# Kernel tuning notes

Measured on AMD Instinct MI355X. Metric: run time of the kernel, lower is better.

Reference implementation:

```python
import jax, jax.numpy as jnp
import numpy as np

MAXDISP = 320
NEG_SLOPE = 0.2


def _lrelu(x):
    return jnp.where(x >= 0, x, NEG_SLOPE * x)


def _conv(x, w, b, stride):
    # NCHW conv, VALID padding (torch Conv2d with padding=0)
    y = jax.lax.conv_general_dilated(x, w, window_strides=stride, padding='VALID',
                                     dimension_numbers=('NCHW', 'OIHW', 'NCHW'))
    return y + b[None, :, None, None]


def _tile_pair(fl, fr, wa, ba, wb, bb):
    # left: 4x4 conv stride (4,4); right: ZeroPad2d((0,3,0,0)) then stride (4,1)
    tl = _lrelu(_conv(_lrelu(_conv(fl, wa, ba, (4, 4))), wb, bb, (1, 1)))
    frp = jnp.pad(fr, ((0, 0), (0, 0), (0, 0), (0, 3)))
    tr = _lrelu(_conv(_lrelu(_conv(frp, wa, ba, (4, 1))), wb, bb, (1, 1)))
    return tl, tr


def _calc_init_disp(fl, fr, D):
    # fl: [B,C,h,w4], fr: [B,C,h,w] with w = 4*w4.
    # grid_sample(nearest, align_corners=True) with integer coords reduces to
    # exact gather at right column index 4*j - d, zero outside (padding_mode=zeros).
    B, C, h, w4 = fl.shape
    w = fr.shape[3]
    j = jnp.arange(w4)
    d = jnp.arange(D)
    idx = 4 * j[None, :] - d[:, None]              # [D, w4]
    valid = idx >= 0                               # only left edge can go OOB
    idxc = jnp.clip(idx, 0, w - 1)
    fr_g = fr[:, :, :, idxc]                       # [B,C,h,D,w4]
    fr_g = jnp.where(valid[None, None, None, :, :], fr_g, jnp.zeros((), fr.dtype))
    cv = jnp.abs(fl[:, :, :, None, :] - fr_g).sum(axis=1)  # L1 over C -> [B,h,D,w4]
    return jnp.transpose(cv, (0, 2, 1, 3))         # [B,D,h,w4]


def _level_hyp(cv, dscrpt_feat, dw, db):
    min_cost = jnp.min(cv, axis=1, keepdims=True)
    disp = jnp.argmin(cv, axis=1, keepdims=True).astype(cv.dtype)
    dscrpt = _lrelu(_conv(jnp.concatenate([min_cost, dscrpt_feat], axis=1), dw, db, (1, 1)))
    z = jnp.zeros_like(disp)
    return jnp.concatenate([disp, z, z, dscrpt], axis=1)  # [B,16,h,w]


def setup_inputs() -> dict:
    key = jax.random.key(0)
    ks = iter(jax.random.split(key, 64))

    def rn(shape, s=1.0):
        return jax.random.normal(next(ks), shape, dtype=jnp.float32) * s

    B, H, W = 1, 384, 1280
    inp = {
        'fea_l16': rn((B, 32, H // 16, W // 16)), 'fea_l8': rn((B, 24, H // 8, W // 8)),
        'fea_l4': rn((B, 24, H // 4, W // 4)), 'fea_l2': rn((B, 16, H // 2, W // 2)),
        'fea_l1': rn((B, 16, H, W)),
        'fea_r16': rn((B, 32, H // 16, W // 16)), 'fea_r8': rn((B, 24, H // 8, W // 8)),
        'fea_r4': rn((B, 24, H // 4, W // 4)), 'fea_r2': rn((B, 16, H // 2, W // 2)),
        'fea_r1': rn((B, 16, H, W)),
    }
    fea_c = {16: 32, 8: 24, 4: 24, 2: 16, 1: 16}
    for s, c in fea_c.items():
        inp[f'tcw{s}a'] = rn((16, c, 4, 4), 0.1)
        inp[f'tcb{s}a'] = rn((16,), 0.1)
        inp[f'tcw{s}b'] = rn((16, 16, 1, 1), 0.1)
        inp[f'tcb{s}b'] = rn((16,), 0.1)
    dsc_in = {16: 17, 8: 17, 4: 33, 2: 25, 1: 25}
    for s, c in dsc_in.items():
        inp[f'dw{s}'] = rn((13, c, 1, 1), 0.1)
        inp[f'db{s}'] = rn((13,), 0.1)
    return inp


def reference(fea_l16, fea_l8, fea_l4, fea_l2, fea_l1,
              fea_r16, fea_r8, fea_r4, fea_r2, fea_r1,
              tcw16a, tcb16a, tcw16b, tcb16b,
              tcw8a, tcb8a, tcw8b, tcb8b,
              tcw4a, tcb4a, tcw4b, tcb4b,
              tcw2a, tcb2a, tcw2b, tcb2b,
              tcw1a, tcb1a, tcw1b, tcb1b,
              dw16, db16, dw8, db8, dw4, db4, dw2, db2, dw1, db1):
    tl16, tr16 = _tile_pair(fea_l16, fea_r16, tcw16a, tcb16a, tcw16b, tcb16b)
    tl8, tr8 = _tile_pair(fea_l8, fea_r8, tcw8a, tcb8a, tcw8b, tcb8b)
    tl4, tr4 = _tile_pair(fea_l4, fea_r4, tcw4a, tcb4a, tcw4b, tcb4b)
    tl2, tr2 = _tile_pair(fea_l2, fea_r2, tcw2a, tcb2a, tcw2b, tcb2b)
    tl1, tr1 = _tile_pair(fea_l1, fea_r1, tcw1a, tcb1a, tcw1b, tcb1b)

    cv16 = _calc_init_disp(tl16, tr16, MAXDISP // 16)
    cv8 = _calc_init_disp(tl8, tr8, MAXDISP // 8)
    cv4 = _calc_init_disp(tl4, tr4, MAXDISP // 4)
    cv2 = _calc_init_disp(tl2, tr2, MAXDISP // 2)
    cv1 = _calc_init_disp(tl1, tr1, MAXDISP)

    hyp16 = _level_hyp(cv16, tl16, dw16, db16)
    hyp8 = _level_hyp(cv8, tl8, dw8, db8)
    hyp4 = _level_hyp(cv4, fea_l16, dw4, db4)
    hyp2 = _level_hyp(cv2, fea_l8, dw2, db2)
    hyp1 = _level_hyp(cv1, fea_l4, dw1, db1)

    return (cv16, cv8, cv4, cv2, cv1, hyp16, hyp8, hyp4, hyp2, hyp1)
```

## Files before the change

kernel.cpp:

```cpp
#include <hip/hip_runtime.h>
#include <float.h>

#define NEG_SLOPE 0.2f

__device__ __forceinline__ float lrelu(float x) { return x >= 0.0f ? x : NEG_SLOPE * x; }

struct ConvSeg {
    const float* in; const float* wa; const float* wb; const float* ba; const float* bb;
    float* out;
    int CIN, H, W, right, nit, npix, blk0;
};
struct ConvTab { ConvSeg seg[10]; };

__global__ __launch_bounds__(256)
void conv_uber(ConvTab tab) {
    __shared__ float s_wa[32 * 256];
    __shared__ float s_wb[256];
    __shared__ float s_ba[16], s_bb[16];

    int si = 0;
#pragma unroll
    for (int i = 1; i < 10; i++) if ((int)blockIdx.x >= tab.seg[i].blk0) si = i;
    const ConvSeg sg = tab.seg[si];
    const int CIN = sg.CIN, W = sg.W, H = sg.H;

    for (int i = threadIdx.x; i < CIN * 256; i += 256)
        s_wa[i] = sg.wa[(i & 15) * (CIN * 16) + (i >> 4)];
    s_wb[threadIdx.x] = sg.wb[(threadIdx.x & 15) * 16 + (threadIdx.x >> 4)];
    if (threadIdx.x < 16) { s_ba[threadIdx.x] = sg.ba[threadIdx.x]; s_bb[threadIdx.x] = sg.bb[threadIdx.x]; }
    __syncthreads();

    int t = ((int)blockIdx.x - sg.blk0) * 256 + threadIdx.x;
    const bool valid = t < sg.nit;
    int ct = valid ? t : sg.nit - 1;

    float m[4][16];
#pragma unroll
    for (int i = 0; i < 4; i++)
#pragma unroll
        for (int co = 0; co < 16; co++) m[i][co] = 0.f;

    int obase;
    if (sg.right) {
        const int W4 = W >> 2;
        int y = ct / W4, xq = ct - y * W4;
        int colb = 4 * xq;
        obase = y * W + colb;
        const float* ib = sg.in + (size_t)(4 * y) * W + colb;
        const bool has1 = colb + 4 < W;
        for (int c = 0; c < CIN; c++) {
            const float* rb = ib + (size_t)c * H * W;
            const float* wc = s_wa + c * 256;
#pragma unroll
            for (int r = 0; r < 4; r++) {
                float4 f0 = *(const float4*)(rb + r * W);
                float4 f1 = make_float4(0.f, 0.f, 0.f, 0.f);
                if (has1) f1 = *(const float4*)(rb + r * W + 4);
                float wv[8] = {f0.x, f0.y, f0.z, f0.w, f1.x, f1.y, f1.z, f1.w};
                const float* wr = wc + r * 64;
#pragma unroll
                for (int kx = 0; kx < 4; kx++) {
                    const float* w2 = wr + kx * 16;
#pragma unroll
                    for (int i = 0; i < 4; i++) {
                        float v = wv[i + kx];
#pragma unroll
                        for (int co = 0; co < 16; co++) m[i][co] = fmaf(v, w2[co], m[i][co]);
                    }
                }
            }
        }
    } else {
        const int OW4 = W >> 4;
        int y = ct / OW4, xg = ct - y * OW4;
        obase = y * (W >> 2) + 4 * xg;
        const float* ib = sg.in + (size_t)(4 * y) * W + 16 * xg;
        for (int c = 0; c < CIN; c++) {
            const float* rb = ib + (size_t)c * H * W;
            const float* wc = s_wa + c * 256;
#pragma unroll
            for (int r = 0; r < 4; r++) {
                float4 v0 = *(const float4*)(rb + r * W);
                float4 v1 = *(const float4*)(rb + r * W + 4);
                float4 v2 = *(const float4*)(rb + r * W + 8);
                float4 v3 = *(const float4*)(rb + r * W + 12);
                float q[4][4] = {{v0.x, v0.y, v0.z, v0.w}, {v1.x, v1.y, v1.z, v1.w},
                                 {v2.x, v2.y, v2.z, v2.w}, {v3.x, v3.y, v3.z, v3.w}};
                const float* wr = wc + r * 64;
#pragma unroll
                for (int kx = 0; kx < 4; kx++) {
                    const float* w2 = wr + kx * 16;
#pragma unroll
                    for (int i = 0; i < 4; i++) {
                        float v = q[i][kx];
#pragma unroll
                        for (int co = 0; co < 16; co++) m[i][co] = fmaf(v, w2[co], m[i][co]);
                    }
                }
            }
        }
    }

    float o[4][16];
#pragma unroll
    for (int i = 0; i < 4; i++) {
#pragma unroll
        for (int co = 0; co < 16; co++) m[i][co] = lrelu(m[i][co] + s_ba[co]);
#pragma unroll
        for (int co = 0; co < 16; co++) o[i][co] = 0.f;
#pragma unroll
        for (int k = 0; k < 16; k++) {
            float mk = m[i][k];
            const float* wr = s_wb + k * 16;
#pragma unroll
            for (int co = 0; co < 16; co++) o[i][co] = fmaf(mk, wr[co], o[i][co]);
        }
    }
    if (valid) {
#pragma unroll
        for (int co = 0; co < 16; co++) {
            float4 v = make_float4(lrelu(o[0][co] + s_bb[co]), lrelu(o[1][co] + s_bb[co]),
                                   lrelu(o[2][co] + s_bb[co]), lrelu(o[3][co] + s_bb[co]));
            *(float4*)(sg.out + (size_t)co * sg.npix + obase) = v;
        }
    }
}

struct CvSeg {
    const float* tl; const float* tr; const float* feat;
    const float* dw; const float* db;
    float* cv; float* hyp;
    int h, w4, w, D, gpc, CF, blk0;
};
struct CvTab { CvSeg seg[5]; };

__global__ __launch_bounds__(256)
void cv_hyp_uber(CvTab tab) {
    __shared__ float smin[256];
    __shared__ int sarg[256];

    int si = 0;
#pragma unroll
    for (int i = 1; i < 5; i++) if ((int)blockIdx.x >= tab.seg[i].blk0) si = i;
    const CvSeg sg = tab.seg[si];

    const int npix = sg.h * sg.w4;
    const int p = threadIdx.x & 15, chunk = threadIdx.x >> 4;
    const int pix = ((int)blockIdx.x - sg.blk0) * 16 + p;
    const bool valid = pix < npix;

    float mloc = FLT_MAX; int aloc = 0;
    if (valid) {
        int y = pix / sg.w4, j = pix - y * sg.w4;
        float tlv[16]; float sumabs = 0.f;
#pragma unroll
        for (int c = 0; c < 16; c++) { tlv[c] = sg.tl[(size_t)c * npix + pix]; sumabs += fabsf(tlv[c]); }

        int ngroups = sg.D >> 2;
        int g0 = chunk * sg.gpc;
        int g1 = min(ngroups, g0 + sg.gpc);
        const float* trrow = sg.tr + (size_t)y * sg.w;
        int hw = sg.h * sg.w;

        float carry[16];
        int b0 = 4 * j - 4 * g0;
        if (g0 < g1 && b0 >= 0) {
#pragma unroll
            for (int c = 0; c < 16; c++) carry[c] = trrow[(size_t)c * hw + b0];
        }
        for (int g = g0; g < g1; g++) {
            int b = 4 * j - 4 * g;
            float a0, a1, a2, a3;
            if (b >= 4) {
                a0 = a1 = a2 = a3 = 0.f;
#pragma unroll
                for (int c = 0; c < 16; c++) {
                    float4 f0 = *(const float4*)(trrow + (size_t)c * hw + (b - 4));
                    float tv = tlv[c];
                    a0 += fabsf(tv - carry[c]);
                    a1 += fabsf(tv - f0.w);
                    a2 += fabsf(tv - f0.z);
                    a3 += fabsf(tv - f0.y);
                    carry[c] = f0.x;
                }
            } else if (b == 0) {
                a0 = 0.f; a1 = a2 = a3 = sumabs;
#pragma unroll
                for (int c = 0; c < 16; c++) a0 += fabsf(tlv[c] - carry[c]);
            } else {
                a0 = a1 = a2 = a3 = sumabs;
            }
            float* cvp = sg.cv + (size_t)(4 * g) * npix + pix;
            cvp[0] = a0; cvp[npix] = a1; cvp[2 * (size_t)npix] = a2; cvp[3 * (size_t)npix] = a3;
            if (a0 < mloc) { mloc = a0; aloc = 4 * g; }
            if (a1 < mloc) { mloc = a1; aloc = 4 * g + 1; }
            if (a2 < mloc) { mloc = a2; aloc = 4 * g + 2; }
            if (a3 < mloc) { mloc = a3; aloc = 4 * g + 3; }
        }
    }
    smin[threadIdx.x] = mloc;
    sarg[threadIdx.x] = aloc;
    __syncthreads();

    if (threadIdx.x < 16 && valid) {
        float mn = smin[threadIdx.x]; int arg = sarg[threadIdx.x];
#pragma unroll
        for (int c2 = 1; c2 < 16; c2++) {
            float v = smin[c2 * 16 + threadIdx.x];
            if (v < mn) { mn = v; arg = sarg[c2 * 16 + threadIdx.x]; }
        }
        float acc[13];
#pragma unroll
        for (int o = 0; o < 13; o++) acc[o] = sg.dw[o * (sg.CF + 1)] * mn;
        for (int c = 0; c < sg.CF; c++) {
            float v = sg.feat[(size_t)c * npix + pix];
#pragma unroll
            for (int o = 0; o < 13; o++) acc[o] = fmaf(v, sg.dw[o * (sg.CF + 1) + 1 + c], acc[o]);
        }
        sg.hyp[pix] = (float)arg;
        sg.hyp[npix + pix] = 0.f;
        sg.hyp[2 * (size_t)npix + pix] = 0.f;
#pragma unroll
        for (int o = 0; o < 13; o++) sg.hyp[(size_t)(3 + o) * npix + pix] = lrelu(acc[o] + sg.db[o]);
    }
}

extern "C" void kernel_launch(void* const* d_in, const int* in_sizes, int n_in,
                              void* d_out, int out_size, void* d_ws, size_t ws_size,
                              hipStream_t stream) {
    (void)in_sizes; (void)n_in; (void)out_size; (void)ws_size;
    float* out = (float*)d_out;
    float* ws = (float*)d_ws;

    const int C[5] = {32, 24, 24, 16, 16};
    const int H[5] = {24, 48, 96, 192, 384};
    const int W[5] = {80, 160, 320, 640, 1280};
    const int D[5] = {20, 40, 80, 160, 320};
    const int wa_i[5] = {10, 14, 18, 22, 26};
    const int dw_i[5] = {30, 32, 34, 36, 38};

    const size_t cv_off[5]  = {0, 2400, 21600, 175200, 1404000};
    const size_t hyp_off[5] = {11234400, 11236320, 11244000, 11274720, 11397600};
    const size_t tl_off[5] = {0, 9600, 48000, 201600, 816000};
    const size_t tr_off[5] = {1920, 17280, 78720, 324480, 1307520};

    const float* fl[5] = {(const float*)d_in[0], (const float*)d_in[1], (const float*)d_in[2],
                          (const float*)d_in[3], (const float*)d_in[4]};
    const float* fr[5] = {(const float*)d_in[5], (const float*)d_in[6], (const float*)d_in[7],
                          (const float*)d_in[8], (const float*)d_in[9]};

    const int ord_lvl[10]  = {4, 4, 3, 3, 2, 2, 1, 1, 0, 0};
    const int ord_side[10] = {1, 0, 1, 0, 1, 0, 1, 0, 1, 0};
    ConvTab ct;
    int blk = 0;
    for (int i = 0; i < 10; i++) {
        int l = ord_lvl[i]; bool right = ord_side[i];
        ConvSeg& s = ct.seg[i];
        s.in = right ? fr[l] : fl[l];
        s.wa = (const float*)d_in[wa_i[l]];
        s.ba = (const float*)d_in[wa_i[l] + 1];
        s.wb = (const float*)d_in[wa_i[l] + 2];
        s.bb = (const float*)d_in[wa_i[l] + 3];
        s.out = ws + (right ? tr_off[l] : tl_off[l]);
        s.CIN = C[l]; s.H = H[l]; s.W = W[l];
        s.right = right ? 1 : 0;
        int OH = H[l] / 4, W4 = W[l] / 4;
        s.nit = right ? OH * W4 : OH * (W4 / 4);
        s.npix = right ? OH * W[l] : OH * W4;
        s.blk0 = blk;
        blk += (s.nit + 255) / 256;
    }
    conv_uber<<<blk, 256, 0, stream>>>(ct);

    const float* feat[5] = {ws + tl_off[0], ws + tl_off[1], fl[0], fl[1], fl[2]};
    const int   CF[5]    = {16, 16, 32, 24, 24};
    CvTab vt;
    blk = 0;
    for (int i = 0; i < 5; i++) {
        int l = 4 - i;
        CvSeg& s = vt.seg[i];
        s.tl = ws + tl_off[l]; s.tr = ws + tr_off[l];
        s.feat = feat[l];
        s.dw = (const float*)d_in[dw_i[l]];
        s.db = (const float*)d_in[dw_i[l] + 1];
        s.cv = out + cv_off[l]; s.hyp = out + hyp_off[l];
        s.h = H[l] / 4; s.w4 = W[l] / 4; s.w = W[l]; s.D = D[l];
        int ngroups = D[l] / 4;
        s.gpc = (ngroups + 15) / 16;
        s.CF = CF[l];
        s.blk0 = blk;
        blk += (s.h * s.w4 + 15) / 16;
    }
    cv_hyp_uber<<<blk, 256, 0, stream>>>(vt);
}
```

Before: 349.8 us.

## Compute one output pixel per thread and read conv weights from global memory

The tile conv kernel drops the shared-memory weight staging and the 4-pixel register blocking. Each thread now computes a single output pixel, reading its inputs with scalar or float4 loads and the weights directly from global memory. This removes the shared-memory fill, the __syncthreads, and register pressure from 4x16 accumulators, so more threads can run at once. In exchange, overlapping input windows in the right-hand branch are no longer reused across pixels, and every thread issues uniform global weight loads, which may become scalar loads or cache traffic.

```diff
diff --git a/kernel.cpp b/kernel.cpp
--- a/kernel.cpp
+++ b/kernel.cpp
@@ -12,118 +12,90 @@
 };
 struct ConvTab { ConvSeg seg[10]; };
 
+__device__ __forceinline__ void accum16(float m[16], const float wv[16],
+                                        const float* __restrict__ wa, int CIN, int c) {
+#pragma unroll
+    for (int co = 0; co < 16; co++) {
+        const float* __restrict__ wc = wa + (size_t)(co * CIN + c) * 16;
+#pragma unroll
+        for (int kk = 0; kk < 16; kk++) m[co] = fmaf(wv[kk], wc[kk], m[co]);
+    }
+}
+
 __global__ __launch_bounds__(256)
 void conv_uber(ConvTab tab) {
-    __shared__ float s_wa[32 * 256];
-    __shared__ float s_wb[256];
-    __shared__ float s_ba[16], s_bb[16];
-
     int si = 0;
 #pragma unroll
     for (int i = 1; i < 10; i++) if ((int)blockIdx.x >= tab.seg[i].blk0) si = i;
     const ConvSeg sg = tab.seg[si];
     const int CIN = sg.CIN, W = sg.W, H = sg.H;
 
-    for (int i = threadIdx.x; i < CIN * 256; i += 256)
-        s_wa[i] = sg.wa[(i & 15) * (CIN * 16) + (i >> 4)];
-    s_wb[threadIdx.x] = sg.wb[(threadIdx.x & 15) * 16 + (threadIdx.x >> 4)];
-    if (threadIdx.x < 16) { s_ba[threadIdx.x] = sg.ba[threadIdx.x]; s_bb[threadIdx.x] = sg.bb[threadIdx.x]; }
-    __syncthreads();
-
-    int t = ((int)blockIdx.x - sg.blk0) * 256 + threadIdx.x;
-    const bool valid = t < sg.nit;
-    int ct = valid ? t : sg.nit - 1;
-
-    float m[4][16];
-#pragma unroll
-    for (int i = 0; i < 4; i++)
-#pragma unroll
-        for (int co = 0; co < 16; co++) m[i][co] = 0.f;
-
-    int obase;
+    const int t = ((int)blockIdx.x - sg.blk0) * 256 + (int)threadIdx.x;
+    if (t >= sg.nit) return;
+
+    const float* __restrict__ wa = sg.wa;
+    float m[16];
+#pragma unroll
+    for (int co = 0; co < 16; co++) m[co] = 0.f;
+
     if (sg.right) {
+        const int y = t / W, x = t - y * W;
+        const float* ib = sg.in + (size_t)(4 * y) * W + x;
+        if (x + 4 <= W) {
+            for (int c = 0; c < CIN; c++) {
+                const float* rb = ib + (size_t)c * H * W;
+                float wv[16];
+#pragma unroll
+                for (int r = 0; r < 4; r++)
+#pragma unroll
+                    for (int k = 0; k < 4; k++) wv[r * 4 + k] = rb[r * W + k];
+                accum16(m, wv, wa, CIN, c);
+            }
+        } else {
+            for (int c = 0; c < CIN; c++) {
+                const float* rb = ib + (size_t)c * H * W;
+                float wv[16];
+#pragma unroll
+                for (int r = 0; r < 4; r++)
+#pragma unroll
+                    for (int k = 0; k < 4; k++) wv[r * 4 + k] = (x + k < W) ? rb[r * W + k] : 0.f;
+                accum16(m, wv, wa, CIN, c);
+            }
+        }
+    } else {
         const int W4 = W >> 2;
-        int y = ct / W4, xq = ct - y * W4;
-        int colb = 4 * xq;
-        obase = y * W + colb;
-        const float* ib = sg.in + (size_t)(4 * y) * W + colb;
-        const bool has1 = colb + 4 < W;
+        const int y = t / W4, x = t - y * W4;
+        const float* ib = sg.in + (size_t)(4 * y) * W + 4 * x;
         for (int c = 0; c < CIN; c++) {
             const float* rb = ib + (size_t)c * H * W;
-            const float* wc = s_wa + c * 256;
+            float wv[16];
 #pragma unroll
             for (int r = 0; r < 4; r++) {
-                float4 f0 = *(const float4*)(rb + r * W);
-                float4 f1 = make_float4(0.f, 0.f, 0.f, 0.f);
-                if (has1) f1 = *(const float4*)(rb + r * W + 4);
-                float wv[8] = {f0.x, f0.y, f0.z, f0.w, f1.x, f1.y, f1.z, f1.w};
-                const float* wr = wc + r * 64;
-#pragma unroll
-                for (int kx = 0; kx < 4; kx++) {
-                    const float* w2 = wr + kx * 16;
-#pragma unroll
-                    for (int i = 0; i < 4; i++) {
-                        float v = wv[i + kx];
-#pragma unroll
-                        for (int co = 0; co < 16; co++) m[i][co] = fmaf(v, w2[co], m[i][co]);
-                    }
-                }
-            }
-        }
-    } else {
-        const int OW4 = W >> 4;
-        int y = ct / OW4, xg = ct - y * OW4;
-        obase = y * (W >> 2) + 4 * xg;
-        const float* ib = sg.in + (size_t)(4 * y) * W + 16 * xg;
-        for (int c = 0; c < CIN; c++) {
-            const float* rb = ib + (size_t)c * H * W;
-            const float* wc = s_wa + c * 256;
-#pragma unroll
-            for (int r = 0; r < 4; r++) {
-                float4 v0 = *(const float4*)(rb + r * W);
-                float4 v1 = *(const float4*)(rb + r * W + 4);
-                float4 v2 = *(const float4*)(rb + r * W + 8);
-                float4 v3 = *(const float4*)(rb + r * W + 12);
-                float q[4][4] = {{v0.x, v0.y, v0.z, v0.w}, {v1.x, v1.y, v1.z, v1.w},
-                                 {v2.x, v2.y, v2.z, v2.w}, {v3.x, v3.y, v3.z, v3.w}};
-                const float* wr = wc + r * 64;
-#pragma unroll
-                for (int kx = 0; kx < 4; kx++) {
-                    const float* w2 = wr + kx * 16;
-#pragma unroll
-                    for (int i = 0; i < 4; i++) {
-                        float v = q[i][kx];
-#pragma unroll
-                        for (int co = 0; co < 16; co++) m[i][co] = fmaf(v, w2[co], m[i][co]);
-                    }
-                }
-            }
-        }
-    }
-
-    float o[4][16];
-#pragma unroll
-    for (int i = 0; i < 4; i++) {
-#pragma unroll
-        for (int co = 0; co < 16; co++) m[i][co] = lrelu(m[i][co] + s_ba[co]);
-#pragma unroll
-        for (int co = 0; co < 16; co++) o[i][co] = 0.f;
-#pragma unroll
-        for (int k = 0; k < 16; k++) {
-            float mk = m[i][k];
-            const float* wr = s_wb + k * 16;
-#pragma unroll
-            for (int co = 0; co < 16; co++) o[i][co] = fmaf(mk, wr[co], o[i][co]);
-        }
-    }
-    if (valid) {
-#pragma unroll
-        for (int co = 0; co < 16; co++) {
-            float4 v = make_float4(lrelu(o[0][co] + s_bb[co]), lrelu(o[1][co] + s_bb[co]),
-                                   lrelu(o[2][co] + s_bb[co]), lrelu(o[3][co] + s_bb[co]));
-            *(float4*)(sg.out + (size_t)co * sg.npix + obase) = v;
-        }
-    }
+                float4 f = *(const float4*)(rb + r * W);
+                wv[r * 4 + 0] = f.x; wv[r * 4 + 1] = f.y;
+                wv[r * 4 + 2] = f.z; wv[r * 4 + 3] = f.w;
+            }
+            accum16(m, wv, wa, CIN, c);
+        }
+    }
+
+    const float* __restrict__ ba = sg.ba;
+    const float* __restrict__ wb = sg.wb;
+    const float* __restrict__ bb = sg.bb;
+#pragma unroll
+    for (int co = 0; co < 16; co++) m[co] = lrelu(m[co] + ba[co]);
+    float o[16];
+#pragma unroll
+    for (int co = 0; co < 16; co++) {
+        const float* __restrict__ wr = wb + co * 16;
+        float a = 0.f;
+#pragma unroll
+        for (int k = 0; k < 16; k++) a = fmaf(m[k], wr[k], a);
+        o[co] = lrelu(a + bb[co]);
+    }
+#pragma unroll
+    for (int co = 0; co < 16; co++)
+        sg.out[(size_t)co * sg.npix + t] = o[co];
 }
 
 struct CvSeg {
@@ -265,8 +237,8 @@
         s.CIN = C[l]; s.H = H[l]; s.W = W[l];
         s.right = right ? 1 : 0;
         int OH = H[l] / 4, W4 = W[l] / 4;
-        s.nit = right ? OH * W4 : OH * (W4 / 4);
-        s.npix = right ? OH * W[l] : OH * W4;
+        s.nit = right ? OH * W[l] : OH * W4;
+        s.npix = s.nit;
         s.blk0 = blk;
         blk += (s.nit + 255) / 256;
     }
```

New measurement: 528.0 us. +51.0%, slower.

## Split conv input channels across blocks with atomic partials and separate epilogue

Applied to the files above, without the earlier changes.

The fused tile conv now splits input channels into slices (2 or 4 per level), and each block accumulates a partial 4x4 conv result into a zeroed workspace with atomicAdd. A new epilogue kernel then applies bias, leaky ReLU, the 1x1 conv and the second activation. The aim is more blocks and less shared memory per block for better occupancy. In exchange it adds a workspace memset, atomic traffic, an extra full read/write pass over the intermediate, and a non-deterministic summation order.

```diff
diff --git a/kernel.cpp b/kernel.cpp
--- a/kernel.cpp
+++ b/kernel.cpp
@@ -6,33 +6,33 @@
 __device__ __forceinline__ float lrelu(float x) { return x >= 0.0f ? x : NEG_SLOPE * x; }
 
 struct ConvSeg {
-    const float* in; const float* wa; const float* wb; const float* ba; const float* bb;
+    const float* in; const float* wa;
     float* out;
-    int CIN, H, W, right, nit, npix, blk0;
+    int CIN, CS, H, W, right, nitpx, npix, bps, blk0;
 };
 struct ConvTab { ConvSeg seg[10]; };
 
-__global__ __launch_bounds__(256)
-void conv_uber(ConvTab tab) {
-    __shared__ float s_wa[32 * 256];
-    __shared__ float s_wb[256];
-    __shared__ float s_ba[16], s_bb[16];
+__global__ __launch_bounds__(256, 3)
+void conv_partial(ConvTab tab) {
+    __shared__ float s_wa[16 * 256];
 
     int si = 0;
 #pragma unroll
     for (int i = 1; i < 10; i++) if ((int)blockIdx.x >= tab.seg[i].blk0) si = i;
     const ConvSeg sg = tab.seg[si];
-    const int CIN = sg.CIN, W = sg.W, H = sg.H;
-
-    for (int i = threadIdx.x; i < CIN * 256; i += 256)
-        s_wa[i] = sg.wa[(i & 15) * (CIN * 16) + (i >> 4)];
-    s_wb[threadIdx.x] = sg.wb[(threadIdx.x & 15) * 16 + (threadIdx.x >> 4)];
-    if (threadIdx.x < 16) { s_ba[threadIdx.x] = sg.ba[threadIdx.x]; s_bb[threadIdx.x] = sg.bb[threadIdx.x]; }
+    const int CIN = sg.CIN, CS = sg.CS, W = sg.W, H = sg.H;
+
+    const int rel = (int)blockIdx.x - sg.blk0;
+    const int slice = rel / sg.bps;
+    const int c0 = slice * CS;
+
+    for (int i = threadIdx.x; i < CS * 256; i += 256)
+        s_wa[i] = sg.wa[(i & 15) * (CIN * 16) + c0 * 16 + (i >> 4)];
     __syncthreads();
 
-    int t = ((int)blockIdx.x - sg.blk0) * 256 + threadIdx.x;
-    const bool valid = t < sg.nit;
-    int ct = valid ? t : sg.nit - 1;
+    const int t = (rel - slice * sg.bps) * 256 + (int)threadIdx.x;
+    const bool valid = t < sg.nitpx;
+    const int ct = valid ? t : sg.nitpx - 1;
 
     float m[4][16];
 #pragma unroll
@@ -40,17 +40,18 @@
 #pragma unroll
         for (int co = 0; co < 16; co++) m[i][co] = 0.f;
 
+    const float* inb = sg.in + (size_t)c0 * H * W;
     int obase;
     if (sg.right) {
         const int W4 = W >> 2;
         int y = ct / W4, xq = ct - y * W4;
         int colb = 4 * xq;
         obase = y * W + colb;
-        const float* ib = sg.in + (size_t)(4 * y) * W + colb;
+        const float* ib = inb + (size_t)(4 * y) * W + colb;
         const bool has1 = colb + 4 < W;
-        for (int c = 0; c < CIN; c++) {
-            const float* rb = ib + (size_t)c * H * W;
-            const float* wc = s_wa + c * 256;
+        for (int cl = 0; cl < CS; cl++) {
+            const float* rb = ib + (size_t)cl * H * W;
+            const float* wc = s_wa + cl * 256;
 #pragma unroll
             for (int r = 0; r < 4; r++) {
                 float4 f0 = *(const float4*)(rb + r * W);
@@ -74,10 +75,10 @@
         const int OW4 = W >> 4;
         int y = ct / OW4, xg = ct - y * OW4;
         obase = y * (W >> 2) + 4 * xg;
-        const float* ib = sg.in + (size_t)(4 * y) * W + 16 * xg;
-        for (int c = 0; c < CIN; c++) {
-            const float* rb = ib + (size_t)c * H * W;
-            const float* wc = s_wa + c * 256;
+        const float* ib = inb + (size_t)(4 * y) * W + 16 * xg;
+        for (int cl = 0; cl < CS; cl++) {
+            const float* rb = ib + (size_t)cl * H * W;
+            const float* wc = s_wa + cl * 256;
 #pragma unroll
             for (int r = 0; r < 4; r++) {
                 float4 v0 = *(const float4*)(rb + r * W);
@@ -101,28 +102,40 @@
         }
     }
 
-    float o[4][16];
-#pragma unroll
-    for (int i = 0; i < 4; i++) {
-#pragma unroll
-        for (int co = 0; co < 16; co++) m[i][co] = lrelu(m[i][co] + s_ba[co]);
-#pragma unroll
-        for (int co = 0; co < 16; co++) o[i][co] = 0.f;
-#pragma unroll
-        for (int k = 0; k < 16; k++) {
-            float mk = m[i][k];
-            const float* wr = s_wb + k * 16;
-#pragma unroll
-            for (int co = 0; co < 16; co++) o[i][co] = fmaf(mk, wr[co], o[i][co]);
-        }
-    }
     if (valid) {
 #pragma unroll
         for (int co = 0; co < 16; co++) {
-            float4 v = make_float4(lrelu(o[0][co] + s_bb[co]), lrelu(o[1][co] + s_bb[co]),
-                                   lrelu(o[2][co] + s_bb[co]), lrelu(o[3][co] + s_bb[co]));
-            *(float4*)(sg.out + (size_t)co * sg.npix + obase) = v;
-        }
+            float* op = sg.out + (size_t)co * sg.npix + obase;
+            atomicAdd(op + 0, m[0][co]);
+            atomicAdd(op + 1, m[1][co]);
+            atomicAdd(op + 2, m[2][co]);
+            atomicAdd(op + 3, m[3][co]);
+        }
+    }
+}
+
+struct EpiSeg { float* buf; const float* ba; const float* wb; const float* bb; int npix, blk0; };
+struct EpiTab { EpiSeg seg[10]; };
+
+__global__ __launch_bounds__(256)
+void conv_epilogue(EpiTab tab) {
+    int si = 0;
+#pragma unroll
+    for (int i = 1; i < 10; i++) if ((int)blockIdx.x >= tab.seg[i].blk0) si = i;
+    const EpiSeg sg = tab.seg[si];
+    const int pix = ((int)blockIdx.x - sg.blk0) * 256 + (int)threadIdx.x;
+    if (pix >= sg.npix) return;
+
+    float x[16];
+#pragma unroll
+    for (int k = 0; k < 16; k++) x[k] = lrelu(sg.buf[(size_t)k * sg.npix + pix] + sg.ba[k]);
+#pragma unroll
+    for (int co = 0; co < 16; co++) {
+        const float* wr = sg.wb + co * 16;
+        float a = 0.f;
+#pragma unroll
+        for (int k = 0; k < 16; k++) a = fmaf(x[k], wr[k], a);
+        sg.buf[(size_t)co * sg.npix + pix] = lrelu(a + sg.bb[co]);
     }
 }
 
@@ -236,6 +249,7 @@
     const int H[5] = {24, 48, 96, 192, 384};
     const int W[5] = {80, 160, 320, 640, 1280};
     const int D[5] = {20, 40, 80, 160, 320};
+    const int S[5] = {2, 2, 2, 4, 4};
     const int wa_i[5] = {10, 14, 18, 22, 26};
     const int dw_i[5] = {30, 32, 34, 36, 38};
 
@@ -249,28 +263,39 @@
     const float* fr[5] = {(const float*)d_in[5], (const float*)d_in[6], (const float*)d_in[7],
                           (const float*)d_in[8], (const float*)d_in[9]};
 
+    hipMemsetAsync(ws, 0, 13094400, stream);
+
     const int ord_lvl[10]  = {4, 4, 3, 3, 2, 2, 1, 1, 0, 0};
     const int ord_side[10] = {1, 0, 1, 0, 1, 0, 1, 0, 1, 0};
     ConvTab ct;
-    int blk = 0;
+    EpiTab et;
+    int blk = 0, eblk = 0;
     for (int i = 0; i < 10; i++) {
         int l = ord_lvl[i]; bool right = ord_side[i];
         ConvSeg& s = ct.seg[i];
         s.in = right ? fr[l] : fl[l];
         s.wa = (const float*)d_in[wa_i[l]];
-        s.ba = (const float*)d_in[wa_i[l] + 1];
-        s.wb = (const float*)d_in[wa_i[l] + 2];
-        s.bb = (const float*)d_in[wa_i[l] + 3];
         s.out = ws + (right ? tr_off[l] : tl_off[l]);
-        s.CIN = C[l]; s.H = H[l]; s.W = W[l];
+        s.CIN = C[l]; s.CS = C[l] / S[l]; s.H = H[l]; s.W = W[l];
         s.right = right ? 1 : 0;
         int OH = H[l] / 4, W4 = W[l] / 4;
-        s.nit = right ? OH * W4 : OH * (W4 / 4);
-        s.npix = right ? OH * W[l] : OH * W4;
+        s.nitpx = right ? OH * W4 : OH * (W4 / 4);
+        s.npix  = right ? OH * W[l] : OH * W4;
+        s.bps = (s.nitpx + 255) / 256;
         s.blk0 = blk;
-        blk += (s.nit + 255) / 256;
-    }
-    conv_uber<<<blk, 256, 0, stream>>>(ct);
+        blk += S[l] * s.bps;
+
+        EpiSeg& e = et.seg[i];
+        e.buf = s.out;
+        e.ba = (const float*)d_in[wa_i[l] + 1];
+        e.wb = (const float*)d_in[wa_i[l] + 2];
+        e.bb = (const float*)d_in[wa_i[l] + 3];
+        e.npix = s.npix;
+        e.blk0 = eblk;
+        eblk += (s.npix + 255) / 256;
+    }
+    conv_partial<<<blk, 256, 0, stream>>>(ct);
+    conv_epilogue<<<eblk, 256, 0, stream>>>(et);
 
     const float* feat[5] = {ws + tl_off[0], ws + tl_off[1], fl[0], fl[1], fl[2]};
     const int   CF[5]    = {16, 16, 32, 24, 24};
```

Result: slower. 676.6 us (+93.5%).
